# Kernel optimization log

Hardware: AMD Instinct MI355X
Metric: run time of the kernel (lower is better)

Reference implementation:

```python
import jax, jax.numpy as jnp
import numpy as np

N_LAYER, N_HEAD, N_EMBD, VOCAB, T_CTX, MAXT, B = 6, 8, 128, 18, 30, 2719, 64


def _ln(x, g, b, eps=1e-5):
    m = x.mean(-1, keepdims=True)
    v = ((x - m) ** 2).mean(-1, keepdims=True)
    return (x - m) * jax.lax.rsqrt(v + eps) * g + b


def setup_inputs() -> dict:
    key = jax.random.key(0)
    ks = iter(jax.random.split(key, 64))
    nrm = lambda shape: jax.random.normal(next(ks), shape, jnp.float32) * 0.02
    E, L4 = N_EMBD, 4 * N_EMBD
    inp = dict(
        states=jax.random.normal(next(ks), (B, T_CTX, 4, 84, 84), jnp.float32),
        actions=jax.random.randint(next(ks), (B, T_CTX, 1), 0, VOCAB),
        rtgs=jax.random.normal(next(ks), (B, T_CTX, 1), jnp.float32),
        timesteps=jax.random.randint(next(ks), (B, 1, 1), 0, MAXT),
        conv_w=nrm((E, 4, 84, 84)),
        class_tok=nrm((1, 1, E)),
        in_proj_w=nrm((3 * E, E)), in_proj_b=jnp.zeros(3 * E),
        out_w=nrm((E, E)), out_b=jnp.zeros(E),
        iln1_g=jnp.ones(E), iln1_b=jnp.zeros(E),
        iln2_g=jnp.ones(E), iln2_b=jnp.zeros(E),
        ffn_w1=nrm((E, E)), ffn_b1=jnp.zeros(E),
        ffn_w2=nrm((E, E)), ffn_b2=jnp.zeros(E),
        ret_w=nrm((E, 1)), ret_b=jnp.zeros(E),
        act_table=nrm((VOCAB, E)),
        pos_emb=nrm((1, 3 * T_CTX + 1, E)),
        global_pos_emb=nrm((1, MAXT + 1, E)),
        ln1_g=jnp.ones((N_LAYER, E)), ln1_b=jnp.zeros((N_LAYER, E)),
        Wq=nrm((N_LAYER, E, E)), bq=jnp.zeros((N_LAYER, E)),
        Wk=nrm((N_LAYER, E, E)), bk=jnp.zeros((N_LAYER, E)),
        Wv=nrm((N_LAYER, E, E)), bv=jnp.zeros((N_LAYER, E)),
        Wo=nrm((N_LAYER, E, E)), bo=jnp.zeros((N_LAYER, E)),
        ln2_g=jnp.ones((N_LAYER, E)), ln2_b=jnp.zeros((N_LAYER, E)),
        W1=nrm((N_LAYER, L4, E)), b1=jnp.zeros((N_LAYER, L4)),
        W2=nrm((N_LAYER, E, L4)), b2=jnp.zeros((N_LAYER, E)),
        lnf_g=jnp.ones(E), lnf_b=jnp.zeros(E),
        head_w=nrm((VOCAB, E)),
    )
    return inp


def _forward(states, actions, rtgs, timesteps, conv_w, class_tok, in_proj_w, in_proj_b,
             out_w, out_b, iln1_g, iln1_b, iln2_g, iln2_b, ffn_w1, ffn_b1, ffn_w2, ffn_b2,
             ret_w, ret_b, act_table, pos_emb, global_pos_emb,
             ln1_g, ln1_b, Wq, bq, Wk, bk, Wv, bv, Wo, bo, ln2_g, ln2_b,
             W1, b1, W2, b2, lnf_g, lnf_b, head_w):
    Bsz, T = states.shape[:2]
    E = conv_w.shape[0]
    H, hd = N_HEAD, E // N_HEAD
    # --- inner TIT: patch embed (kernel 84 = frame size -> single patch = one big dot) ---
    obs = states.reshape(Bsz * T, *states.shape[2:])                      # (BT,4,84,84)
    patch = jnp.einsum('bchw,echw->be', obs, conv_w)[:, None, :]          # (BT,1,E)
    x = jnp.concatenate([jnp.broadcast_to(class_tok, (Bsz * T, 1, E)), patch], axis=1)  # (BT,2,E)
    h = _ln(x, iln1_g, iln1_b)
    q, k, v = jnp.split(h @ in_proj_w.T + in_proj_b, 3, axis=-1)
    att = jax.nn.softmax(jnp.einsum('bqe,bke->bqk', q, k) / jnp.sqrt(jnp.float32(E)), axis=-1)
    x = x + jnp.einsum('bqk,bke->bqe', att, v) @ out_w.T + out_b
    h2 = _ln(x, iln2_g, iln2_b)
    x = x + jax.nn.relu(h2 @ ffn_w1.T + ffn_b1) @ ffn_w2.T + ffn_b2
    state_emb = x[:, 0, :].reshape(Bsz, T, E)                             # class token
    # --- token interleave (targets=None path -> length 3T-1, last T-1 actions) ---
    rtg_emb = jnp.tanh(rtgs @ ret_w.T + ret_b)                            # (B,T,E)
    act_emb = jnp.tanh(act_table[actions[..., 0]])                        # (B,T,E)
    Lt = 3 * T - 1
    tok = jnp.zeros((Bsz, Lt, E), states.dtype)
    tok = tok.at[:, 0::3].set(rtg_emb).at[:, 1::3].set(state_emb).at[:, 2::3].set(act_emb[:, 1:])
    pos = global_pos_emb[0][timesteps[:, 0, 0]][:, None, :] + pos_emb[:, :Lt, :]
    x = tok + pos
    # --- outer causal GPT blocks ---
    mask = jnp.tril(jnp.ones((Lt, Lt), bool))
    for i in range(N_LAYER):
        hh = _ln(x, ln1_g[i], ln1_b[i])
        proj = lambda w, b: (hh @ w.T + b).reshape(Bsz, Lt, H, hd).transpose(0, 2, 1, 3)
        q, k, v = proj(Wq[i], bq[i]), proj(Wk[i], bk[i]), proj(Wv[i], bv[i])
        att = jnp.einsum('bhqd,bhkd->bhqk', q, k) / jnp.sqrt(jnp.float32(hd))
        att = jax.nn.softmax(jnp.where(mask, att, -jnp.inf), axis=-1)
        y = jnp.einsum('bhqk,bhkd->bhqd', att, v).transpose(0, 2, 1, 3).reshape(Bsz, Lt, E)
        x = x + y @ Wo[i].T + bo[i]
        hh2 = _ln(x, ln2_g[i], ln2_b[i])
        x = x + jax.nn.gelu(hh2 @ W1[i].T + b1[i], approximate=False) @ W2[i].T + b2[i]
    logits = _ln(x, lnf_g, lnf_b) @ head_w.T
    return logits[:, 1::3, :]                                             # (B,T,vocab) state-position logits


def reference(states, actions, rtgs, timesteps, conv_w, class_tok, in_proj_w, in_proj_b,
              out_w, out_b, iln1_g, iln1_b, iln2_g, iln2_b, ffn_w1, ffn_b1, ffn_w2, ffn_b2,
              ret_w, ret_b, act_table, pos_emb, global_pos_emb,
              ln1_g, ln1_b, Wq, bq, Wk, bk, Wv, bv, Wo, bo, ln2_g, ln2_b,
              W1, b1, W2, b2, lnf_g, lnf_b, head_w):
    return _forward(states, actions, rtgs, timesteps, conv_w, class_tok, in_proj_w, in_proj_b,
                    out_w, out_b, iln1_g, iln1_b, iln2_g, iln2_b, ffn_w1, ffn_b1, ffn_w2, ffn_b2,
                    ret_w, ret_b, act_table, pos_emb, global_pos_emb,
                    ln1_g, ln1_b, Wq, bq, Wk, bk, Wv, bv, Wo, bo, ln2_g, ln2_b,
                    W1, b1, W2, b2, lnf_g, lnf_b, head_w)
```

## Files before the change

kernel.cpp:

```cpp
#include <hip/hip_runtime.h>

#define NB   64
#define NT   30
#define NBT  1920
#define EE   128
#define KP   28224
#define LTK  89
#define NS   5696
#define NLY  6
#define NV   18
#define NZ   21

typedef unsigned short ushort_t;
using bf16x8 = __attribute__((ext_vector_type(8))) short;
using us8    = __attribute__((ext_vector_type(8))) unsigned short;
using f32x4  = __attribute__((ext_vector_type(4))) float;
using f32x16 = __attribute__((ext_vector_type(16))) float;

__device__ inline ushort_t f2bf(float f){
  union { float f; unsigned u; } v; v.f = f;
  unsigned r = v.u + 0x7FFFu + ((v.u >> 16) & 1u);
  return (ushort_t)(r >> 16);
}

__global__ __launch_bounds__(256) void wcvt(
  const float* conv, const float* Wq, const float* Wk, const float* Wv,
  const float* Wo, const float* W1, const float* W2,
  const float* in_w, const float* out_w, const float* f1w, const float* f2w,
  const float* bq, const float* bk, const float* bv,
  ushort_t* dc, ushort_t* dqkv, ushort_t* dout, ushort_t* d1, ushort_t* d2,
  ushort_t* dinw, ushort_t* doutw, ushort_t* df1, ushort_t* df2, float* bqkv)
{
  if (blockIdx.x >= 4776){
    int idx = (blockIdx.x-4776)*256 + threadIdx.x;
    if (idx < NLY*128){ int l=idx>>7, j=idx&127;
      bqkv[l*384+j]=bq[idx]; bqkv[l*384+128+j]=bk[idx]; bqkv[l*384+256+j]=bv[idx]; }
    return;
  }
  long i = 4l*((long)blockIdx.x*256 + threadIdx.x);
  if (i >= 3612672l && i < 3907584l){
    long o = i - 3612672l;
    int  seg = (int)(o / 98304l);
    long off2 = o - (long)seg*98304l;
    long layer = off2 >> 14, rem = off2 & 16383l;
    const float* s = (seg==0) ? Wq : (seg==1) ? Wk : Wv;
    float4 f = *reinterpret_cast<const float4*>(s+off2);
    long dst = layer*49152l + (long)seg*16384l + rem;
    dqkv[dst]=f2bf(f.x); dqkv[dst+1]=f2bf(f.y); dqkv[dst+2]=f2bf(f.z); dqkv[dst+3]=f2bf(f.w);
    return;
  }
  const float* s; ushort_t* d; long off;
  if      (i < 3612672l){ s=conv;  d=dc;    off=i; }
  else if (i < 4005888l){ s=Wo;    d=dout;  off=i-3907584l; }
  else if (i < 4399104l){ s=W1;    d=d1;    off=i-4005888l; }
  else if (i < 4792320l){ s=W2;    d=d2;    off=i-4399104l; }
  else if (i < 4841472l){ s=in_w;  d=dinw;  off=i-4792320l; }
  else if (i < 4857856l){ s=out_w; d=doutw; off=i-4841472l; }
  else if (i < 4874240l){ s=f1w;   d=df1;   off=i-4857856l; }
  else                  { s=f2w;   d=df2;   off=i-4874240l; }
  float4 f = *reinterpret_cast<const float4*>(s+off);
  d[off]=f2bf(f.x); d[off+1]=f2bf(f.y); d[off+2]=f2bf(f.z); d[off+3]=f2bf(f.w);
}

__global__ __launch_bounds__(256) void patch_gemm(
  const float* __restrict__ A, const ushort_t* __restrict__ Wb, float* __restrict__ C)
{
  __shared__ __align__(16) ushort_t As[64*64];
  __shared__ __align__(16) ushort_t Ws[128*64];
  const int tid = threadIdx.x, lane = tid & 63, wid = tid >> 6;
  const int m0 = blockIdx.x * 64;
  const int kbase = blockIdx.z * 1344;
  float* Cz = C + (size_t)blockIdx.z * NBT * EE;
  const int ra = tid>>2, ca = (tid&3)*16, swa = (ra&7)<<3;
  const int rw = tid>>1, cw = (tid&1)*32, sww = (rw&7)<<3;
  const float*    Ab = A  + (size_t)(m0+ra)*KP + kbase + ca;
  const ushort_t* Wp = Wb + (size_t)rw*KP  + kbase + cw;
  f32x4 acc[8];
  #pragma unroll
  for (int j=0;j<8;j++) acc[j] = (f32x4){0.f,0.f,0.f,0.f};
  float4 fa[4]; us8 wr[4];
  #pragma unroll
  for (int q=0;q<4;q++) fa[q] = *reinterpret_cast<const float4*>(Ab + 4*q);
  #pragma unroll
  for (int q=0;q<4;q++) wr[q] = *reinterpret_cast<const us8*>(Wp + 8*q);

  for (int kt = 0; kt < 21; ++kt){
    { us8 o0, o1;
      o0[0]=f2bf(fa[0].x); o0[1]=f2bf(fa[0].y); o0[2]=f2bf(fa[0].z); o0[3]=f2bf(fa[0].w);
      o0[4]=f2bf(fa[1].x); o0[5]=f2bf(fa[1].y); o0[6]=f2bf(fa[1].z); o0[7]=f2bf(fa[1].w);
      o1[0]=f2bf(fa[2].x); o1[1]=f2bf(fa[2].y); o1[2]=f2bf(fa[2].z); o1[3]=f2bf(fa[2].w);
      o1[4]=f2bf(fa[3].x); o1[5]=f2bf(fa[3].y); o1[6]=f2bf(fa[3].z); o1[7]=f2bf(fa[3].w);
      *reinterpret_cast<us8*>(&As[ra*64 + ( ca    ^ swa)]) = o0;
      *reinterpret_cast<us8*>(&As[ra*64 + ((ca+8) ^ swa)]) = o1;
      #pragma unroll
      for (int q=0;q<4;q++)
        *reinterpret_cast<us8*>(&Ws[rw*64 + ((cw+8*q) ^ sww)]) = wr[q];
    }
    if (kt < 20){
      #pragma unroll
      for (int q=0;q<4;q++) fa[q] = *reinterpret_cast<const float4*>(Ab + (kt+1)*64 + 4*q);
      #pragma unroll
      for (int q=0;q<4;q++) wr[q] = *reinterpret_cast<const us8*>(Wp + (kt+1)*64 + 8*q);
    }
    __syncthreads();
    #pragma unroll
    for (int ks=0; ks<2; ++ks){
      int arow = wid*16 + (lane&15);
      int kb = ks*32 + (lane>>4)*8;
      bf16x8 a = *reinterpret_cast<const bf16x8*>(&As[arow*64 + (kb ^ ((arow&7)<<3))]);
      #pragma unroll
      for (int nt=0; nt<8; ++nt){
        int nn = nt*16 + (lane&15);
        bf16x8 b = *reinterpret_cast<const bf16x8*>(&Ws[nn*64 + (kb ^ ((nn&7)<<3))]);
        acc[nt] = __builtin_amdgcn_mfma_f32_16x16x32_bf16(a, b, acc[nt], 0,0,0);
      }
    }
    __syncthreads();
  }
  #pragma unroll
  for (int nt=0; nt<8; ++nt)
    #pragma unroll
    for (int rr=0;rr<4;rr++){
      int row = m0 + wid*16 + (lane>>4)*4 + rr;
      int col = nt*16 + (lane&15);
      Cz[row*EE + col] = acc[nt][rr];
    }
}

__global__ __launch_bounds__(256, 1) void inner_tit(
  const float* __restrict__ part, const float* __restrict__ ctok,
  const ushort_t* __restrict__ inw, const float* __restrict__ in_b,
  const ushort_t* __restrict__ outw, const float* __restrict__ out_b,
  const float* __restrict__ g1, const float* __restrict__ b1_,
  const float* __restrict__ g2, const float* __restrict__ b2_,
  const ushort_t* __restrict__ f1wb, const float* __restrict__ fb1,
  const ushort_t* __restrict__ f2wb, const float* __restrict__ fb2,
  const float* __restrict__ rtgs, const int* __restrict__ actions,
  const int* __restrict__ tsteps, const float* __restrict__ ret_w,
  const float* __restrict__ ret_b, const float* __restrict__ act_tab,
  const float* __restrict__ pos_emb, const float* __restrict__ gpos,
  const float* __restrict__ ln1g0, const float* __restrict__ ln1b0,
  float* __restrict__ x, ushort_t* __restrict__ xln)
{
  __shared__ __align__(16) ushort_t wbuf[384*128];
  __shared__ float xs[16*128];
  __shared__ __align__(16) ushort_t hb[16*128];
  __shared__ __align__(16) ushort_t hf[16*128];
  __shared__ float qkv[16*384];
  __shared__ float ssm[32];
  const int tid = threadIdx.x, lane = tid & 63, wid = tid >> 6;
  const int bt0 = blockIdx.x * 8;

  auto stageWB = [&](const ushort_t* src, int R, int rowoff){
    for (int c = tid; c < R*16; c += 256){
      int rr = c >> 4, cc = (c & 15) * 8;
      *reinterpret_cast<us8*>(&wbuf[(rowoff+rr)*128 + (cc ^ ((rr&7)<<3))]) =
        *reinterpret_cast<const us8*>(src + (size_t)rr*128 + cc);
    }
  };
  auto lnrow = [&](const float* gam, const float* bet, ushort_t* dst){
    int r = tid >> 4, e0 = (tid & 15) * 8;
    float v[8];
    #pragma unroll
    for (int j=0;j<8;j++) v[j] = xs[r*128 + e0 + j];
    float s = 0;
    #pragma unroll
    for (int j=0;j<8;j++) s += v[j];
    s += __shfl_xor(s,1); s += __shfl_xor(s,2); s += __shfl_xor(s,4); s += __shfl_xor(s,8);
    float mean = s * (1.0f/128.0f);
    float vs = 0;
    #pragma unroll
    for (int j=0;j<8;j++){ float d = v[j]-mean; vs += d*d; }
    vs += __shfl_xor(vs,1); vs += __shfl_xor(vs,2); vs += __shfl_xor(vs,4); vs += __shfl_xor(vs,8);
    float rstd = rsqrtf(vs*(1.0f/128.0f) + 1e-5f);
    us8 o;
    #pragma unroll
    for (int j=0;j<8;j++) o[j] = f2bf((v[j]-mean)*rstd*gam[e0+j] + bet[e0+j]);
    *reinterpret_cast<us8*>(&dst[r*128 + (e0 ^ ((r&7)<<3))]) = o;
  };

  { int r = tid >> 4, e0 = (tid & 15) * 8;
    float v[8];
    if ((r & 1) == 0){
      #pragma unroll
      for (int j=0;j<8;j++) v[j] = ctok[e0+j];
    } else {
      #pragma unroll
      for (int j=0;j<8;j++) v[j] = 0.f;
      int bt = bt0 + (r>>1);
      for (int z=0; z<NZ; ++z){
        const float* p = part + (size_t)z*NBT*EE + (size_t)bt*128 + e0;
        float4 f0 = *reinterpret_cast<const float4*>(p);
        float4 f1 = *reinterpret_cast<const float4*>(p+4);
        v[0]+=f0.x; v[1]+=f0.y; v[2]+=f0.z; v[3]+=f0.w;
        v[4]+=f1.x; v[5]+=f1.y; v[6]+=f1.z; v[7]+=f1.w;
      }
    }
    #pragma unroll
    for (int j=0;j<8;j++) xs[r*128 + e0 + j] = v[j];
  }
  stageWB(inw, 384, 0);
  __syncthreads();

  lnrow(g1, b1_, hb);
  __syncthreads();

  { int al = lane & 15, kq = (lane>>4)*8;
    #pragma unroll
    for (int j=0;j<6;++j){
      int nt = wid*6 + j;
      f32x4 acc = (f32x4){0.f,0.f,0.f,0.f};
      int nrow = nt*16 + al, nsw = (nrow&7)<<3;
      #pragma unroll
      for (int ks=0; ks<4; ++ks){
        int kb = ks*32 + kq;
        bf16x8 a = *reinterpret_cast<const bf16x8*>(&hb[al*128 + (kb ^ ((al&7)<<3))]);
        bf16x8 b = *reinterpret_cast<const bf16x8*>(&wbuf[nrow*128 + (kb ^ nsw)]);
        acc = __builtin_amdgcn_mfma_f32_16x16x32_bf16(a, b, acc, 0,0,0);
      }
      float bia = in_b[nt*16 + al];
      #pragma unroll
      for (int rr=0; rr<4; ++rr){
        int row = (lane>>4)*4 + rr;
        qkv[row*384 + nt*16 + al] = acc[rr] + bia;
      }
    }
  }
  __syncthreads();

  { int d = tid >> 3, j = tid & 7;
    int i = d >> 2, p = d & 3;
    const float* qp = &qkv[(2*i + (p>>1))*384 + j*16];
    const float* kp = &qkv[(2*i + (p&1))*384 + 128 + j*16];
    float s = 0;
    #pragma unroll
    for (int e=0;e<16;e++) s += qp[e]*kp[e];
    s += __shfl_xor(s,1); s += __shfl_xor(s,2); s += __shfl_xor(s,4);
    if (j == 0) ssm[d] = s;
  }
  stageWB(outw, 128, 0);
  stageWB(f1wb, 128, 128);
  stageWB(f2wb, 128, 256);
  __syncthreads();

  { int r = tid >> 4, e0 = (tid & 15)*8;
    int i = r >> 1, t = r & 1;
    const float sc = 0.08838834764831845f;
    float s0 = ssm[i*4 + t*2]*sc, s1 = ssm[i*4 + t*2 + 1]*sc;
    float m = fmaxf(s0,s1), p0 = __expf(s0-m), p1 = __expf(s1-m);
    float iv = 1.0f/(p0+p1); p0 *= iv; p1 *= iv;
    const float* v0 = &qkv[(2*i)*384 + 256 + e0];
    const float* v1 = &qkv[(2*i+1)*384 + 256 + e0];
    us8 o;
    #pragma unroll
    for (int j=0;j<8;j++) o[j] = f2bf(p0*v0[j] + p1*v1[j]);
    *reinterpret_cast<us8*>(&hb[r*128 + (e0 ^ ((r&7)<<3))]) = o;
  }
  __syncthreads();

  { int al = lane & 15, kq = (lane>>4)*8;
    #pragma unroll
    for (int j=0;j<2;++j){
      int nt = wid*2 + j;
      f32x4 acc = (f32x4){0.f,0.f,0.f,0.f};
      int nrow = nt*16 + al, nsw = (nrow&7)<<3;
      #pragma unroll
      for (int ks=0; ks<4; ++ks){
        int kb = ks*32 + kq;
        bf16x8 a = *reinterpret_cast<const bf16x8*>(&hb[al*128 + (kb ^ ((al&7)<<3))]);
        bf16x8 b = *reinterpret_cast<const bf16x8*>(&wbuf[nrow*128 + (kb ^ nsw)]);
        acc = __builtin_amdgcn_mfma_f32_16x16x32_bf16(a, b, acc, 0,0,0);
      }
      float bia = out_b[nt*16 + al];
      #pragma unroll
      for (int rr=0; rr<4; ++rr){
        int row = (lane>>4)*4 + rr;
        xs[row*128 + nt*16 + al] += acc[rr] + bia;
      }
    }
  }
  __syncthreads();

  lnrow(g2, b2_, hb);
  __syncthreads();

  { int al = lane & 15, kq = (lane>>4)*8;
    #pragma unroll
    for (int j=0;j<2;++j){
      int nt = wid*2 + j;
      f32x4 acc = (f32x4){0.f,0.f,0.f,0.f};
      int nrow = nt*16 + al, nsw = (nrow&7)<<3;
      #pragma unroll
      for (int ks=0; ks<4; ++ks){
        int kb = ks*32 + kq;
        bf16x8 a = *reinterpret_cast<const bf16x8*>(&hb[al*128 + (kb ^ ((al&7)<<3))]);
        bf16x8 b = *reinterpret_cast<const bf16x8*>(&wbuf[(128+nrow)*128 + (kb ^ nsw)]);
        acc = __builtin_amdgcn_mfma_f32_16x16x32_bf16(a, b, acc, 0,0,0);
      }
      float bia = fb1[nt*16 + al];
      #pragma unroll
      for (int rr=0; rr<4; ++rr){
        int row = (lane>>4)*4 + rr;
        hf[row*128 + ((nt*16+al) ^ ((row&7)<<3))] = f2bf(fmaxf(acc[rr] + bia, 0.f));
      }
    }
  }
  __syncthreads();

  { int al = lane & 15, kq = (lane>>4)*8;
    #pragma unroll
    for (int j=0;j<2;++j){
      int nt = wid*2 + j;
      f32x4 acc = (f32x4){0.f,0.f,0.f,0.f};
      int nrow = nt*16 + al, nsw = (nrow&7)<<3;
      #pragma unroll
      for (int ks=0; ks<4; ++ks){
        int kb = ks*32 + kq;
        bf16x8 a = *reinterpret_cast<const bf16x8*>(&hf[al*128 + (kb ^ ((al&7)<<3))]);
        bf16x8 b = *reinterpret_cast<const bf16x8*>(&wbuf[(256+nrow)*128 + (kb ^ nsw)]);
        acc = __builtin_amdgcn_mfma_f32_16x16x32_bf16(a, b, acc, 0,0,0);
      }
      float bia = fb2[nt*16 + al];
      #pragma unroll
      for (int rr=0; rr<4; ++rr){
        int row = (lane>>4)*4 + rr;
        xs[row*128 + nt*16 + al] += acc[rr] + bia;
      }
    }
  }
  __syncthreads();

  { int q = tid >> 3, j = tid & 7;
    if (q < 24){
      int i = q / 3, kind = q - 3*i;
      int btg = bt0 + i, b = btg / NT, t = btg - b*NT;
      bool valid = !(kind == 2 && t == 0);
      if (valid){
        int prow = (kind==0) ? 3*t : (kind==1) ? 3*t+1 : 3*t-1;
        size_t xrow = ((size_t)b*LTK + prow)*128;
        int ts = tsteps[b];
        int e0 = j*16;
        float v[16];
        if (kind == 1){
          #pragma unroll
          for (int e=0;e<16;e++) v[e] = xs[(2*i)*128 + e0 + e];
        } else if (kind == 0){
          float rv = rtgs[b*NT+t];
          #pragma unroll
          for (int e=0;e<16;e++) v[e] = tanhf(rv*ret_w[e0+e] + ret_b[e0+e]);
        } else {
          int a = actions[b*NT+t];
          #pragma unroll
          for (int e=0;e<16;e++) v[e] = tanhf(act_tab[a*128 + e0 + e]);
        }
        #pragma unroll
        for (int e=0;e<16;e++)
          v[e] += gpos[(size_t)ts*128 + e0 + e] + pos_emb[prow*128 + e0 + e];
        #pragma unroll
        for (int e=0;e<16;e++) x[xrow + e0 + e] = v[e];
        float s = 0;
        #pragma unroll
        for (int e=0;e<16;e++) s += v[e];
        s += __shfl_xor(s,1); s += __shfl_xor(s,2); s += __shfl_xor(s,4);
        float mean = s * (1.0f/128.0f);
        float vs = 0;
        #pragma unroll
        for (int e=0;e<16;e++){ float d = v[e]-mean; vs += d*d; }
        vs += __shfl_xor(vs,1); vs += __shfl_xor(vs,2); vs += __shfl_xor(vs,4);
        float rstd = rsqrtf(vs*(1.0f/128.0f) + 1e-5f);
        #pragma unroll
        for (int e=0;e<16;e++)
          xln[xrow + e0 + e] = f2bf((v[e]-mean)*rstd*ln1g0[e0+e] + ln1b0[e0+e]);
      }
    }
  }
}

__global__ __launch_bounds__(256, 2) void attn_fused(
  const ushort_t* __restrict__ xln, const ushort_t* __restrict__ Wqkv,
  const float* __restrict__ bqkv, ushort_t* __restrict__ y)
{
  __shared__ __align__(16) char sm[69504];
  ushort_t* ab  = (ushort_t*)sm;
  ushort_t* wb  = (ushort_t*)(sm + 24576);
  float*    S   = (float*)sm;
  ushort_t* qa  = (ushort_t*)(sm + 37248);
  ushort_t* ka  = (ushort_t*)(sm + 41472);
  ushort_t* vta = (ushort_t*)(sm + 45696);
  ushort_t* pb  = (ushort_t*)(sm + 49152);
  float*    inv = (float*)(sm + 69120);

  const int b = blockIdx.x >> 3, h = blockIdx.x & 7;
  const int tid = threadIdx.x, lane = tid & 63, wid = tid >> 6;

  for (int idx = tid; idx < 1536; idx += 256){
    int row = idx >> 4, c0 = (idx & 15) * 8;
    us8 v;
    if (row < LTK) v = *reinterpret_cast<const us8*>(xln + ((size_t)(b*LTK+row))*128 + c0);
    else           v = (us8){0,0,0,0,0,0,0,0};
    *reinterpret_cast<us8*>(&ab[row*128 + (c0 ^ ((row&7)<<3))]) = v;
  }
  for (int idx = tid; idx < 384; idx += 256){
    int rr = idx >> 3, c = (idx & 7) * 16;
    int seg = rr >> 4, n = rr & 15;
    const ushort_t* src = Wqkv + (size_t)(seg*128 + h*16 + n)*128 + c;
    int sw = (rr&7)<<3;
    *reinterpret_cast<us8*>(&wb[rr*128 + ( c    ^ sw)]) = *reinterpret_cast<const us8*>(src);
    *reinterpret_cast<us8*>(&wb[rr*128 + ((c+8) ^ sw)]) = *reinterpret_cast<const us8*>(src+8);
  }
  __syncthreads();

  for (int idx = wid; idx < 18; idx += 4){
    int rt = idx / 3, nt = idx - 3*(idx/3);
    f32x4 acc = (f32x4){0.f,0.f,0.f,0.f};
    int arow = rt*16 + (lane&15), asw = (arow&7)<<3;
    int nrow = nt*16 + (lane&15), nsw = (nrow&7)<<3;
    #pragma unroll
    for (int ks=0; ks<4; ++ks){
      int kb = ks*32 + (lane>>4)*8;
      bf16x8 a = *reinterpret_cast<const bf16x8*>(&ab[arow*128 + (kb ^ asw)]);
      bf16x8 bf = *reinterpret_cast<const bf16x8*>(&wb[nrow*128 + (kb ^ nsw)]);
      acc = __builtin_amdgcn_mfma_f32_16x16x32_bf16(a, bf, acc, 0,0,0);
    }
    int d = lane & 15;
    float bia = bqkv[nt*128 + h*16 + d];
    #pragma unroll
    for (int rr=0; rr<4; ++rr){
      int rg = rt*16 + (lane>>4)*4 + rr;
      ushort_t hv = f2bf(acc[rr] + bia);
      if      (nt == 0) qa[rg*22 + d] = hv;
      else if (nt == 1) ka[rg*22 + d] = hv;
      else              vta[d*108 + rg] = hv;
    }
  }
  __syncthreads();

  {
    static const int TR[6] = {0,1,1,2,2,2};
    static const int TC[6] = {0,0,1,0,1,2};
    for (int idx = wid; idx < 6; idx += 4){
      int R = TR[idx], C = TC[idx];
      int arow = R*32 + (lane&31), brow = C*32 + (lane&31);
      int ke = (lane>>5)*8;
      bf16x8 a  = *reinterpret_cast<const bf16x8*>(&qa[arow*22 + ke]);
      bf16x8 bf = *reinterpret_cast<const bf16x8*>(&ka[brow*22 + ke]);
      f32x16 sc = {};
      sc = __builtin_amdgcn_mfma_f32_32x32x16_bf16(a, bf, sc, 0,0,0);
      #pragma unroll
      for (int r=0; r<16; ++r){
        int rin = (r&3) + 8*(r>>2) + 4*(lane>>5);
        S[(R*32+rin)*97 + C*32 + (lane&31)] = sc[r]*0.25f;
      }
    }
  }
  __syncthreads();

  if (tid < 192){
    int t = tid >> 1, half = tid & 1;
    int u0 = half*48;
    float mx = -1e30f;
    if (t < LTK){
      for (int u=u0; u<u0+48; ++u) if (u<=t) mx = fmaxf(mx, S[t*97+u]);
    }
    mx = fmaxf(mx, __shfl_xor(mx,1));
    float smv = 0;
    if (t < LTK){
      for (int u=u0; u<u0+48; ++u){
        float p = 0;
        if (u<=t){ p = __expf(S[t*97+u]-mx); smv += p; }
        pb[t*104+u] = f2bf(p);
      }
    } else {
      for (int u=u0; u<u0+48; ++u) pb[t*104+u] = 0;
    }
    smv += __shfl_xor(smv,1);
    if (half==0) inv[t] = (t<LTK) ? 1.0f/smv : 0.0f;
  }
  __syncthreads();

  for (int rt = wid; rt < 6; rt += 4){
    int arow = rt*16 + (lane&15);
    f32x4 acc = (f32x4){0.f,0.f,0.f,0.f};
    #pragma unroll
    for (int ks=0; ks<3; ++ks){
      int kb = ks*32 + (lane>>4)*8;
      bf16x8 a  = *reinterpret_cast<const bf16x8*>(&pb[arow*104 + kb]);
      bf16x8 bf = *reinterpret_cast<const bf16x8*>(&vta[(lane&15)*108 + kb]);
      acc = __builtin_amdgcn_mfma_f32_16x16x32_bf16(a, bf, acc, 0,0,0);
    }
    #pragma unroll
    for (int rr=0; rr<4; ++rr){
      int rg = rt*16 + (lane>>4)*4 + rr;
      if (rg < LTK)
        y[(size_t)(b*LTK+rg)*128 + h*16 + (lane&15)] = f2bf(acc[rr]*inv[rg]);
    }
  }
}

template<bool HEAD>
__global__ __launch_bounds__(256, 2) void ffn_fused(
  const ushort_t* __restrict__ yg, const ushort_t* __restrict__ Wo,
  const float* __restrict__ bo, const float* __restrict__ g2,
  const float* __restrict__ b2g, const ushort_t* __restrict__ W1,
  const float* __restrict__ b1v, const ushort_t* __restrict__ W2,
  const float* __restrict__ b2v, float* __restrict__ x,
  const float* __restrict__ lnng, const float* __restrict__ lnnb,
  ushort_t* __restrict__ xlnout,
  const float* __restrict__ lnfg, const float* __restrict__ lnfb,
  const float* __restrict__ hw, float* __restrict__ out)
{
  __shared__ __align__(16) char sm[66304];
  ushort_t* wbs = (ushort_t*)sm;
  float*    xr  = (float*)(sm + 32768);
  ushort_t* h2  = (ushort_t*)(sm + 49664);
  ushort_t* f1  = (ushort_t*)(sm + 57856);
  const int tid = threadIdx.x, lane = tid & 63, wid = tid >> 6;
  const int m0 = blockIdx.x * 32;

  auto stageW = [&](const ushort_t* src_base, size_t stride, int buf){
    int rr = tid >> 2, q = tid & 3, sw = (rr&7)<<3;
    const ushort_t* s = src_base + (size_t)rr*stride + q*32;
    ushort_t* d = wbs + buf*8192 + rr*128;
    #pragma unroll
    for (int g=0; g<4; ++g)
      *reinterpret_cast<us8*>(&d[(q*32+g*8) ^ sw]) =
        *reinterpret_cast<const us8*>(s + g*8);
  };
  auto gemmT = [&](const ushort_t* abuf, int buf, f32x4* accp){
    int nrow = wid*16 + (lane&15), nsw = (nrow&7)<<3;
    const ushort_t* wbp = wbs + buf*8192;
    #pragma unroll
    for (int rt=0; rt<2; ++rt){
      int arow = rt*16 + (lane&15), asw = (arow&7)<<3;
      #pragma unroll
      for (int ks=0; ks<4; ++ks){
        int kb = ks*32 + (lane>>4)*8;
        bf16x8 a = *reinterpret_cast<const bf16x8*>(&abuf[arow*128 + (kb ^ asw)]);
        bf16x8 bb = *reinterpret_cast<const bf16x8*>(&wbp[nrow*128 + (kb ^ nsw)]);
        accp[rt] = __builtin_amdgcn_mfma_f32_16x16x32_bf16(a, bb, accp[rt], 0,0,0);
      }
    }
  };

  { int rr = tid>>3, q = tid&7, sw = (rr&7)<<3;
    const ushort_t* src = yg + (size_t)(m0+rr)*128 + q*16;
    *reinterpret_cast<us8*>(&f1[rr*128 + ((q*16)   ^ sw)]) = *reinterpret_cast<const us8*>(src);
    *reinterpret_cast<us8*>(&f1[rr*128 + ((q*16+8) ^ sw)]) = *reinterpret_cast<const us8*>(src+8);
  }
  stageW(Wo, 128, 0);
  __syncthreads();
  f32x4 accA[2][2];
  #pragma unroll
  for (int s_=0;s_<2;++s_){ accA[s_][0]=(f32x4){0,0,0,0}; accA[s_][1]=(f32x4){0,0,0,0}; }
  stageW(Wo + 64*128, 128, 1);
  gemmT(f1, 0, accA[0]);
  __syncthreads();
  gemmT(f1, 1, accA[1]);
  #pragma unroll
  for (int s_=0; s_<2; ++s_){
    int col = s_*64 + wid*16 + (lane&15);
    float bia = bo[col];
    #pragma unroll
    for (int rt=0; rt<2; ++rt)
      #pragma unroll
      for (int rr=0; rr<4; ++rr){
        int row = rt*16 + (lane>>4)*4 + rr;
        xr[row*132 + col] = accA[s_][rt][rr] + bia + x[(size_t)(m0+row)*128 + col];
      }
  }
  __syncthreads();

  { int r = tid>>3, q = tid&7;
    float xv[16];
    #pragma unroll
    for (int i=0;i<16;i++) xv[i] = xr[r*132 + q*16 + i];
    float s = 0;
    #pragma unroll
    for (int i=0;i<16;i++) s += xv[i];
    s += __shfl_xor(s,1); s += __shfl_xor(s,2); s += __shfl_xor(s,4);
    float mean = s * (1.0f/128.0f);
    float vs = 0;
    #pragma unroll
    for (int i=0;i<16;i++){ float d = xv[i]-mean; vs += d*d; }
    vs += __shfl_xor(vs,1); vs += __shfl_xor(vs,2); vs += __shfl_xor(vs,4);
    float rstd = rsqrtf(vs*(1.0f/128.0f) + 1e-5f);
    int sw = (r&7)<<3;
    #pragma unroll
    for (int g=0; g<2; ++g){
      us8 o;
      #pragma unroll
      for (int j=0;j<8;j++){
        int c = q*16 + g*8 + j;
        o[j] = f2bf((xv[g*8+j]-mean)*rstd*g2[c] + b2g[c]);
      }
      *reinterpret_cast<us8*>(&h2[r*128 + ((q*16+g*8) ^ sw)]) = o;
    }
  }
  stageW(W1, 128, 0);
  __syncthreads();

  f32x4 acc2[2][2];
  #pragma unroll
  for (int s_=0;s_<2;++s_){ acc2[s_][0]=(f32x4){0,0,0,0}; acc2[s_][1]=(f32x4){0,0,0,0}; }
  int buf = 0;
  for (int c=0; c<4; ++c){
    stageW(W1 + (size_t)(c*128+64)*128, 128, buf^1);
    { f32x4 ac[2] = {(f32x4){0,0,0,0},(f32x4){0,0,0,0}};
      gemmT(h2, buf, ac);
      int cl = wid*16 + (lane&15);
      float bia = b1v[c*128 + cl];
      #pragma unroll
      for (int rt=0; rt<2; ++rt)
        #pragma unroll
        for (int rr=0; rr<4; ++rr){
          int row = rt*16 + (lane>>4)*4 + rr;
          float v = ac[rt][rr] + bia;
          v = 0.5f*v*(1.0f + erff(v*0.70710678118654752f));
          f1[row*128 + (cl ^ ((row&7)<<3))] = f2bf(v);
        }
    }
    __syncthreads();
    stageW(W2 + (size_t)c*128, 512, buf);
    { f32x4 ac[2] = {(f32x4){0,0,0,0},(f32x4){0,0,0,0}};
      gemmT(h2, buf^1, ac);
      int cl = 64 + wid*16 + (lane&15);
      float bia = b1v[c*128 + cl];
      #pragma unroll
      for (int rt=0; rt<2; ++rt)
        #pragma unroll
        for (int rr=0; rr<4; ++rr){
          int row = rt*16 + (lane>>4)*4 + rr;
          float v = ac[rt][rr] + bia;
          v = 0.5f*v*(1.0f + erff(v*0.70710678118654752f));
          f1[row*128 + (cl ^ ((row&7)<<3))] = f2bf(v);
        }
    }
    __syncthreads();
    stageW(W2 + (size_t)64*512 + (size_t)c*128, 512, buf^1);
    gemmT(f1, buf, acc2[0]);
    __syncthreads();
    if (c < 3) stageW(W1 + (size_t)((c+1)*128)*128, 128, buf);
    gemmT(f1, buf^1, acc2[1]);
    __syncthreads();
  }

  #pragma unroll
  for (int s_=0; s_<2; ++s_){
    int col = s_*64 + wid*16 + (lane&15);
    float bia = b2v[col];
    #pragma unroll
    for (int rt=0; rt<2; ++rt)
      #pragma unroll
      for (int rr=0; rr<4; ++rr){
        int row = rt*16 + (lane>>4)*4 + rr;
        float v = acc2[s_][rt][rr] + bia + xr[row*132 + col];
        xr[row*132 + col] = v;
        if constexpr (!HEAD) x[(size_t)(m0+row)*128 + col] = v;
      }
  }
  __syncthreads();
  if constexpr (!HEAD){
    int r = tid>>3, q = tid&7;
    float xv[16];
    #pragma unroll
    for (int i=0;i<16;i++) xv[i] = xr[r*132 + q*16 + i];
    float s = 0;
    #pragma unroll
    for (int i=0;i<16;i++) s += xv[i];
    s += __shfl_xor(s,1); s += __shfl_xor(s,2); s += __shfl_xor(s,4);
    float mean = s * (1.0f/128.0f);
    float vs = 0;
    #pragma unroll
    for (int i=0;i<16;i++){ float d = xv[i]-mean; vs += d*d; }
    vs += __shfl_xor(vs,1); vs += __shfl_xor(vs,2); vs += __shfl_xor(vs,4);
    float rstd = rsqrtf(vs*(1.0f/128.0f) + 1e-5f);
    #pragma unroll
    for (int g=0; g<2; ++g){
      us8 o;
      #pragma unroll
      for (int j=0;j<8;j++){
        int c = q*16 + g*8 + j;
        o[j] = f2bf((xv[g*8+j]-mean)*rstd*lnng[c] + lnnb[c]);
      }
      *reinterpret_cast<us8*>(xlnout + (size_t)(m0+r)*128 + q*16 + g*8) = o;
    }
  } else {
    for (int r = wid; r < 32; r += 4){
      int s = m0 + r, b = s / LTK, p = s - b*LTK;
      if (p % 3 != 1) continue;
      int t = p / 3;
      float v1 = xr[r*132 + lane];
      float v2 = xr[r*132 + 64 + lane];
      float sum = v1 + v2;
      sum += __shfl_xor(sum,1); sum += __shfl_xor(sum,2); sum += __shfl_xor(sum,4);
      sum += __shfl_xor(sum,8); sum += __shfl_xor(sum,16); sum += __shfl_xor(sum,32);
      float mean = sum*(1.0f/128.0f);
      float d1 = v1-mean, d2 = v2-mean;
      float var = d1*d1 + d2*d2;
      var += __shfl_xor(var,1); var += __shfl_xor(var,2); var += __shfl_xor(var,4);
      var += __shfl_xor(var,8); var += __shfl_xor(var,16); var += __shfl_xor(var,32);
      float rstd = rsqrtf(var*(1.0f/128.0f) + 1e-5f);
      float h1 = d1*rstd*lnfg[lane]    + lnfb[lane];
      float h2v= d2*rstd*lnfg[lane+64] + lnfb[lane+64];
      #pragma unroll
      for (int o=0; o<NV; ++o){
        float sdot = h1*hw[o*128+lane] + h2v*hw[o*128+lane+64];
        sdot += __shfl_xor(sdot,1); sdot += __shfl_xor(sdot,2); sdot += __shfl_xor(sdot,4);
        sdot += __shfl_xor(sdot,8); sdot += __shfl_xor(sdot,16); sdot += __shfl_xor(sdot,32);
        if (lane == 0) out[(size_t)(b*NT+t)*NV + o] = sdot;
      }
    }
  }
}

extern "C" void kernel_launch(void* const* d_in, const int* in_sizes, int n_in,
                              void* d_out, int out_size, void* d_ws, size_t ws_size,
                              hipStream_t stream)
{
  const float* states  = (const float*)d_in[0];
  const int*   actions = (const int*)  d_in[1];
  const float* rtgs    = (const float*)d_in[2];
  const int*   tsteps  = (const int*)  d_in[3];
  const float* conv_w  = (const float*)d_in[4];
  const float* ctok    = (const float*)d_in[5];
  const float* in_w    = (const float*)d_in[6];
  const float* in_b    = (const float*)d_in[7];
  const float* out_w   = (const float*)d_in[8];
  const float* out_b   = (const float*)d_in[9];
  const float* i1g     = (const float*)d_in[10];
  const float* i1b     = (const float*)d_in[11];
  const float* i2g     = (const float*)d_in[12];
  const float* i2b     = (const float*)d_in[13];
  const float* fw1     = (const float*)d_in[14];
  const float* fb1     = (const float*)d_in[15];
  const float* fw2     = (const float*)d_in[16];
  const float* fb2     = (const float*)d_in[17];
  const float* ret_w   = (const float*)d_in[18];
  const float* ret_b   = (const float*)d_in[19];
  const float* act_tab = (const float*)d_in[20];
  const float* pos_emb = (const float*)d_in[21];
  const float* gpos    = (const float*)d_in[22];
  const float* ln1g    = (const float*)d_in[23];
  const float* ln1b    = (const float*)d_in[24];
  const float* Wq      = (const float*)d_in[25];
  const float* bq      = (const float*)d_in[26];
  const float* Wk      = (const float*)d_in[27];
  const float* bk      = (const float*)d_in[28];
  const float* Wv      = (const float*)d_in[29];
  const float* bv      = (const float*)d_in[30];
  const float* Wo      = (const float*)d_in[31];
  const float* bo      = (const float*)d_in[32];
  const float* ln2g    = (const float*)d_in[33];
  const float* ln2b    = (const float*)d_in[34];
  const float* W1      = (const float*)d_in[35];
  const float* b1      = (const float*)d_in[36];
  const float* W2      = (const float*)d_in[37];
  const float* b2      = (const float*)d_in[38];
  const float* lnfg    = (const float*)d_in[39];
  const float* lnfb    = (const float*)d_in[40];
  const float* head_w  = (const float*)d_in[41];

  char* w = (char*)d_ws;
  size_t off = 0;
  auto alloc = [&](size_t bytes)->char* {
    char* p = w + off; off += (bytes + 255) & ~(size_t)255; return p;
  };
  float*    part  = (float*)   alloc((size_t)NZ*NBT*EE*4);
  float*    x     = (float*)   alloc((size_t)NS*EE*4);
  ushort_t* xln   = (ushort_t*)alloc((size_t)NS*EE*2);
  ushort_t* yb    = (ushort_t*)alloc((size_t)NS*EE*2);
  ushort_t* cwb   = (ushort_t*)alloc((size_t)EE*KP*2);
  ushort_t* Wqkvb = (ushort_t*)alloc((size_t)NLY*384*128*2);
  ushort_t* Wob   = (ushort_t*)alloc((size_t)NLY*128*128*2);
  ushort_t* W1b   = (ushort_t*)alloc((size_t)NLY*512*128*2);
  ushort_t* W2b   = (ushort_t*)alloc((size_t)NLY*128*512*2);
  ushort_t* inwb  = (ushort_t*)alloc((size_t)384*128*2);
  ushort_t* outwb = (ushort_t*)alloc((size_t)128*128*2);
  ushort_t* f1wb  = (ushort_t*)alloc((size_t)128*128*2);
  ushort_t* f2wb  = (ushort_t*)alloc((size_t)128*128*2);
  float*    bqkv  = (float*)   alloc(NLY*384*4);
  (void)in_sizes; (void)n_in; (void)out_size; (void)ws_size;

  wcvt<<<4779,256,0,stream>>>(conv_w,Wq,Wk,Wv,Wo,W1,W2,
                              in_w,out_w,fw1,fw2, bq,bk,bv,
                              cwb,Wqkvb,Wob,W1b,W2b,
                              inwb,outwb,f1wb,f2wb, bqkv);
  patch_gemm<<<dim3(30,1,NZ),256,0,stream>>>(states, cwb, part);
  inner_tit<<<240,256,0,stream>>>(part, ctok, inwb, in_b, outwb, out_b,
                                  i1g,i1b,i2g,i2b, f1wb,fb1, f2wb,fb2,
                                  rtgs, actions, tsteps, ret_w, ret_b, act_tab,
                                  pos_emb, gpos, ln1g, ln1b, x, xln);
  for (int i=0;i<NLY;i++){
    attn_fused<<<512,256,0,stream>>>(
      xln, Wqkvb+(size_t)i*49152, bqkv+(size_t)i*384, yb);
    if (i < NLY-1)
      ffn_fused<false><<<178,256,0,stream>>>(
        yb, Wob+(size_t)i*16384, bo+i*128, ln2g+i*128, ln2b+i*128,
        W1b+(size_t)i*65536, b1+i*512, W2b+(size_t)i*65536, b2+i*128, x,
        ln1g+(i+1)*128, ln1b+(i+1)*128, xln,
        nullptr, nullptr, nullptr, nullptr);
    else
      ffn_fused<true><<<178,256,0,stream>>>(
        yb, Wob+(size_t)i*16384, bo+i*128, ln2g+i*128, ln2b+i*128,
        W1b+(size_t)i*65536, b1+i*512, W2b+(size_t)i*65536, b2+i*128, x,
        nullptr, nullptr, nullptr,
        lnfg, lnfb, head_w, (float*)d_out);
  }
}
```

Measured before the change: 341.8 us.

## Fuse attention and FFN into one per-layer kernel with ping-pong LN buffers

```diff
diff --git a/kernel.cpp b/kernel.cpp
--- a/kernel.cpp
+++ b/kernel.cpp
@@ -376,151 +376,151 @@
   }
 }
 
-__global__ __launch_bounds__(256, 2) void attn_fused(
-  const ushort_t* __restrict__ xln, const ushort_t* __restrict__ Wqkv,
-  const float* __restrict__ bqkv, ushort_t* __restrict__ y)
-{
-  __shared__ __align__(16) char sm[69504];
-  ushort_t* ab  = (ushort_t*)sm;
-  ushort_t* wb  = (ushort_t*)(sm + 24576);
-  float*    S   = (float*)sm;
-  ushort_t* qa  = (ushort_t*)(sm + 37248);
-  ushort_t* ka  = (ushort_t*)(sm + 41472);
-  ushort_t* vta = (ushort_t*)(sm + 45696);
-  ushort_t* pb  = (ushort_t*)(sm + 49152);
-  float*    inv = (float*)(sm + 69120);
-
-  const int b = blockIdx.x >> 3, h = blockIdx.x & 7;
-  const int tid = threadIdx.x, lane = tid & 63, wid = tid >> 6;
-
-  for (int idx = tid; idx < 1536; idx += 256){
-    int row = idx >> 4, c0 = (idx & 15) * 8;
-    us8 v;
-    if (row < LTK) v = *reinterpret_cast<const us8*>(xln + ((size_t)(b*LTK+row))*128 + c0);
-    else           v = (us8){0,0,0,0,0,0,0,0};
-    *reinterpret_cast<us8*>(&ab[row*128 + (c0 ^ ((row&7)<<3))]) = v;
-  }
-  for (int idx = tid; idx < 384; idx += 256){
-    int rr = idx >> 3, c = (idx & 7) * 16;
-    int seg = rr >> 4, n = rr & 15;
-    const ushort_t* src = Wqkv + (size_t)(seg*128 + h*16 + n)*128 + c;
-    int sw = (rr&7)<<3;
-    *reinterpret_cast<us8*>(&wb[rr*128 + ( c    ^ sw)]) = *reinterpret_cast<const us8*>(src);
-    *reinterpret_cast<us8*>(&wb[rr*128 + ((c+8) ^ sw)]) = *reinterpret_cast<const us8*>(src+8);
-  }
-  __syncthreads();
-
-  for (int idx = wid; idx < 18; idx += 4){
-    int rt = idx / 3, nt = idx - 3*(idx/3);
-    f32x4 acc = (f32x4){0.f,0.f,0.f,0.f};
-    int arow = rt*16 + (lane&15), asw = (arow&7)<<3;
-    int nrow = nt*16 + (lane&15), nsw = (nrow&7)<<3;
-    #pragma unroll
-    for (int ks=0; ks<4; ++ks){
-      int kb = ks*32 + (lane>>4)*8;
-      bf16x8 a = *reinterpret_cast<const bf16x8*>(&ab[arow*128 + (kb ^ asw)]);
-      bf16x8 bf = *reinterpret_cast<const bf16x8*>(&wb[nrow*128 + (kb ^ nsw)]);
-      acc = __builtin_amdgcn_mfma_f32_16x16x32_bf16(a, bf, acc, 0,0,0);
-    }
-    int d = lane & 15;
-    float bia = bqkv[nt*128 + h*16 + d];
-    #pragma unroll
-    for (int rr=0; rr<4; ++rr){
-      int rg = rt*16 + (lane>>4)*4 + rr;
-      ushort_t hv = f2bf(acc[rr] + bia);
-      if      (nt == 0) qa[rg*22 + d] = hv;
-      else if (nt == 1) ka[rg*22 + d] = hv;
-      else              vta[d*108 + rg] = hv;
-    }
-  }
-  __syncthreads();
-
-  {
-    static const int TR[6] = {0,1,1,2,2,2};
-    static const int TC[6] = {0,0,1,0,1,2};
-    for (int idx = wid; idx < 6; idx += 4){
-      int R = TR[idx], C = TC[idx];
-      int arow = R*32 + (lane&31), brow = C*32 + (lane&31);
-      int ke = (lane>>5)*8;
-      bf16x8 a  = *reinterpret_cast<const bf16x8*>(&qa[arow*22 + ke]);
-      bf16x8 bf = *reinterpret_cast<const bf16x8*>(&ka[brow*22 + ke]);
-      f32x16 sc = {};
-      sc = __builtin_amdgcn_mfma_f32_32x32x16_bf16(a, bf, sc, 0,0,0);
-      #pragma unroll
-      for (int r=0; r<16; ++r){
-        int rin = (r&3) + 8*(r>>2) + 4*(lane>>5);
-        S[(R*32+rin)*97 + C*32 + (lane&31)] = sc[r]*0.25f;
-      }
-    }
-  }
-  __syncthreads();
-
-  if (tid < 192){
-    int t = tid >> 1, half = tid & 1;
-    int u0 = half*48;
-    float mx = -1e30f;
-    if (t < LTK){
-      for (int u=u0; u<u0+48; ++u) if (u<=t) mx = fmaxf(mx, S[t*97+u]);
-    }
-    mx = fmaxf(mx, __shfl_xor(mx,1));
-    float smv = 0;
-    if (t < LTK){
-      for (int u=u0; u<u0+48; ++u){
-        float p = 0;
-        if (u<=t){ p = __expf(S[t*97+u]-mx); smv += p; }
-        pb[t*104+u] = f2bf(p);
-      }
-    } else {
-      for (int u=u0; u<u0+48; ++u) pb[t*104+u] = 0;
-    }
-    smv += __shfl_xor(smv,1);
-    if (half==0) inv[t] = (t<LTK) ? 1.0f/smv : 0.0f;
-  }
-  __syncthreads();
-
-  for (int rt = wid; rt < 6; rt += 4){
-    int arow = rt*16 + (lane&15);
-    f32x4 acc = (f32x4){0.f,0.f,0.f,0.f};
-    #pragma unroll
-    for (int ks=0; ks<3; ++ks){
-      int kb = ks*32 + (lane>>4)*8;
-      bf16x8 a  = *reinterpret_cast<const bf16x8*>(&pb[arow*104 + kb]);
-      bf16x8 bf = *reinterpret_cast<const bf16x8*>(&vta[(lane&15)*108 + kb]);
-      acc = __builtin_amdgcn_mfma_f32_16x16x32_bf16(a, bf, acc, 0,0,0);
-    }
-    #pragma unroll
-    for (int rr=0; rr<4; ++rr){
-      int rg = rt*16 + (lane>>4)*4 + rr;
-      if (rg < LTK)
-        y[(size_t)(b*LTK+rg)*128 + h*16 + (lane&15)] = f2bf(acc[rr]*inv[rg]);
-    }
-  }
-}
-
 template<bool HEAD>
-__global__ __launch_bounds__(256, 2) void ffn_fused(
-  const ushort_t* __restrict__ yg, const ushort_t* __restrict__ Wo,
-  const float* __restrict__ bo, const float* __restrict__ g2,
-  const float* __restrict__ b2g, const ushort_t* __restrict__ W1,
-  const float* __restrict__ b1v, const ushort_t* __restrict__ W2,
-  const float* __restrict__ b2v, float* __restrict__ x,
+__global__ __launch_bounds__(256, 2) void layer_fused(
+  const ushort_t* __restrict__ xln, float* __restrict__ x,
+  const ushort_t* __restrict__ Wqkv, const float* __restrict__ bqkv,
+  const ushort_t* __restrict__ Wo, const float* __restrict__ bo,
+  const float* __restrict__ g2, const float* __restrict__ b2g,
+  const ushort_t* __restrict__ W1, const float* __restrict__ b1v,
+  const ushort_t* __restrict__ W2, const float* __restrict__ b2v,
   const float* __restrict__ lnng, const float* __restrict__ lnnb,
   ushort_t* __restrict__ xlnout,
   const float* __restrict__ lnfg, const float* __restrict__ lnfb,
   const float* __restrict__ hw, float* __restrict__ out)
 {
-  __shared__ __align__(16) char sm[66304];
-  ushort_t* wbs = (ushort_t*)sm;
+  __shared__ __align__(16) char sm[73088];
+  ushort_t* kln = (ushort_t*)sm;
+  ushort_t* wb  = (ushort_t*)(sm + 24576);
+  ushort_t* qa  = (ushort_t*)(sm + 36864);
+  ushort_t* ka  = (ushort_t*)(sm + 38272);
+  ushort_t* vta = (ushort_t*)(sm + 42496);
+  float*    S   = (float*)(sm + 45824);
+  ushort_t* pb  = (ushort_t*)(sm + 58112);
+  float*    inv = (float*)(sm + 64768);
+  ushort_t* yb  = (ushort_t*)(sm + 64896);
+  ushort_t* wdb = (ushort_t*)sm;
   float*    xr  = (float*)(sm + 32768);
   ushort_t* h2  = (ushort_t*)(sm + 49664);
-  ushort_t* f1  = (ushort_t*)(sm + 57856);
+  ushort_t* f1  = (ushort_t*)(sm + 64896);
+
   const int tid = threadIdx.x, lane = tid & 63, wid = tid >> 6;
-  const int m0 = blockIdx.x * 32;
+  const int b = blockIdx.x / 3, j = blockIdx.x % 3;
+  const int R0 = j*32;
+  const int P  = (j==2) ? LTK : R0 + 32;
+  const int SR = R0 + 32;
+  const int PT16 = (P+15)>>4, PT32 = (P+31)>>5;
+  const int VR = (j==2) ? (LTK-64) : 32;
+  const int m0g = b*LTK + R0;
+
+  for (int idx = tid; idx < SR*16; idx += 256){
+    int row = idx >> 4, c0 = (idx & 15)*8;
+    us8 v;
+    if (row < LTK) v = *reinterpret_cast<const us8*>(xln + ((size_t)(b*LTK+row))*128 + c0);
+    else           v = (us8){0,0,0,0,0,0,0,0};
+    *reinterpret_cast<us8*>(&kln[row*128 + (c0 ^ ((row&7)<<3))]) = v;
+  }
+  __syncthreads();
+
+  for (int h = 0; h < 8; ++h){
+    for (int idx = tid; idx < 384; idx += 256){
+      int rr = idx >> 3, c = (idx & 7)*16;
+      int seg = rr >> 4, n = rr & 15;
+      const ushort_t* src = Wqkv + (size_t)(seg*128 + h*16 + n)*128 + c;
+      int sw = (rr&7)<<3;
+      *reinterpret_cast<us8*>(&wb[rr*128 + ( c    ^ sw)]) = *reinterpret_cast<const us8*>(src);
+      *reinterpret_cast<us8*>(&wb[rr*128 + ((c+8) ^ sw)]) = *reinterpret_cast<const us8*>(src+8);
+    }
+    __syncthreads();
+    { int NU = 2 + 2*PT16;
+      for (int u = wid; u < NU; u += 4){
+        int typ, rt;
+        if (u < 2)            { typ = 0; rt = u; }
+        else if (u < 2+PT16)  { typ = 1; rt = u-2; }
+        else                  { typ = 2; rt = u-2-PT16; }
+        int al = lane & 15;
+        int arow = ((typ==0)? R0 : 0) + rt*16 + al;
+        int asw = (arow&7)<<3;
+        int nrow = typ*16 + al, nsw = (nrow&7)<<3;
+        f32x4 acc = (f32x4){0.f,0.f,0.f,0.f};
+        #pragma unroll
+        for (int ks=0; ks<4; ++ks){
+          int kb = ks*32 + (lane>>4)*8;
+          bf16x8 a  = *reinterpret_cast<const bf16x8*>(&kln[arow*128 + (kb ^ asw)]);
+          bf16x8 bf = *reinterpret_cast<const bf16x8*>(&wb[nrow*128 + (kb ^ nsw)]);
+          acc = __builtin_amdgcn_mfma_f32_16x16x32_bf16(a, bf, acc, 0,0,0);
+        }
+        float bia = bqkv[typ*128 + h*16 + al];
+        #pragma unroll
+        for (int rr=0; rr<4; ++rr){
+          int rg = rt*16 + (lane>>4)*4 + rr;
+          ushort_t hv = f2bf(acc[rr] + bia);
+          if      (typ == 0) qa[rg*22 + al] = hv;
+          else if (typ == 1) ka[rg*22 + al] = hv;
+          else               vta[al*104 + rg] = hv;
+        }
+      }
+    }
+    __syncthreads();
+    for (int ct = wid; ct < PT32; ct += 4){
+      int ke = (lane>>5)*8;
+      bf16x8 a  = *reinterpret_cast<const bf16x8*>(&qa[(lane&31)*22 + ke]);
+      bf16x8 bf = *reinterpret_cast<const bf16x8*>(&ka[(ct*32+(lane&31))*22 + ke]);
+      f32x16 sc = {};
+      sc = __builtin_amdgcn_mfma_f32_32x32x16_bf16(a, bf, sc, 0,0,0);
+      #pragma unroll
+      for (int r=0; r<16; ++r){
+        int rin = (r&3) + 8*(r>>2) + 4*(lane>>5);
+        S[rin*96 + ct*32 + (lane&31)] = sc[r]*0.25f;
+      }
+    }
+    __syncthreads();
+    { int r = tid >> 3, q8 = tid & 7;
+      int tg = R0 + r, u0 = q8*12, lim = PT32*32;
+      float sv[12];
+      float mx = -1e30f;
+      #pragma unroll
+      for (int k=0;k<12;k++){
+        int u = u0+k;
+        float s = (u < lim && u <= tg) ? S[r*96+u] : -1e30f;
+        sv[k] = s; mx = fmaxf(mx, s);
+      }
+      mx = fmaxf(mx, __shfl_xor(mx,1));
+      mx = fmaxf(mx, __shfl_xor(mx,2));
+      mx = fmaxf(mx, __shfl_xor(mx,4));
+      float sum = 0;
+      #pragma unroll
+      for (int k=0;k<12;k++){
+        float p = (sv[k] > -1e29f) ? __expf(sv[k]-mx) : 0.f;
+        sum += p;
+        pb[r*104 + u0 + k] = f2bf(p);
+      }
+      sum += __shfl_xor(sum,1); sum += __shfl_xor(sum,2); sum += __shfl_xor(sum,4);
+      if (q8 == 0) inv[r] = 1.0f/sum;
+    }
+    __syncthreads();
+    for (int rt = wid; rt < 2; rt += 4){
+      int arow = rt*16 + (lane&15);
+      f32x4 acc = (f32x4){0.f,0.f,0.f,0.f};
+      for (int ks=0; ks<PT32; ++ks){
+        int kb = ks*32 + (lane>>4)*8;
+        bf16x8 a  = *reinterpret_cast<const bf16x8*>(&pb[arow*104 + kb]);
+        bf16x8 bf = *reinterpret_cast<const bf16x8*>(&vta[(lane&15)*104 + kb]);
+        acc = __builtin_amdgcn_mfma_f32_16x16x32_bf16(a, bf, acc, 0,0,0);
+      }
+      #pragma unroll
+      for (int rr=0; rr<4; ++rr){
+        int row = rt*16 + (lane>>4)*4 + rr;
+        yb[row*128 + ((h*16+(lane&15)) ^ ((row&7)<<3))] = f2bf(acc[rr]*inv[row]);
+      }
+    }
+    __syncthreads();
+  }
 
   auto stageW = [&](const ushort_t* src_base, size_t stride, int buf){
     int rr = tid >> 2, q = tid & 3, sw = (rr&7)<<3;
     const ushort_t* s = src_base + (size_t)rr*stride + q*32;
-    ushort_t* d = wbs + buf*8192 + rr*128;
+    ushort_t* d = wdb + buf*8192 + rr*128;
     #pragma unroll
     for (int g=0; g<4; ++g)
       *reinterpret_cast<us8*>(&d[(q*32+g*8) ^ sw]) =
@@ -528,34 +528,29 @@
   };
   auto gemmT = [&](const ushort_t* abuf, int buf, f32x4* accp){
     int nrow = wid*16 + (lane&15), nsw = (nrow&7)<<3;
-    const ushort_t* wbp = wbs + buf*8192;
+    const ushort_t* wbp = wdb + buf*8192;
     #pragma unroll
     for (int rt=0; rt<2; ++rt){
       int arow = rt*16 + (lane&15), asw = (arow&7)<<3;
       #pragma unroll
       for (int ks=0; ks<4; ++ks){
         int kb = ks*32 + (lane>>4)*8;
-        bf16x8 a = *reinterpret_cast<const bf16x8*>(&abuf[arow*128 + (kb ^ asw)]);
+        bf16x8 a  = *reinterpret_cast<const bf16x8*>(&abuf[arow*128 + (kb ^ asw)]);
         bf16x8 bb = *reinterpret_cast<const bf16x8*>(&wbp[nrow*128 + (kb ^ nsw)]);
         accp[rt] = __builtin_amdgcn_mfma_f32_16x16x32_bf16(a, bb, accp[rt], 0,0,0);
       }
     }
   };
 
-  { int rr = tid>>3, q = tid&7, sw = (rr&7)<<3;
-    const ushort_t* src = yg + (size_t)(m0+rr)*128 + q*16;
-    *reinterpret_cast<us8*>(&f1[rr*128 + ((q*16)   ^ sw)]) = *reinterpret_cast<const us8*>(src);
-    *reinterpret_cast<us8*>(&f1[rr*128 + ((q*16+8) ^ sw)]) = *reinterpret_cast<const us8*>(src+8);
-  }
   stageW(Wo, 128, 0);
   __syncthreads();
   f32x4 accA[2][2];
   #pragma unroll
   for (int s_=0;s_<2;++s_){ accA[s_][0]=(f32x4){0,0,0,0}; accA[s_][1]=(f32x4){0,0,0,0}; }
   stageW(Wo + 64*128, 128, 1);
-  gemmT(f1, 0, accA[0]);
-  __syncthreads();
-  gemmT(f1, 1, accA[1]);
+  gemmT(yb, 0, accA[0]);
+  __syncthreads();
+  gemmT(yb, 1, accA[1]);
   #pragma unroll
   for (int s_=0; s_<2; ++s_){
     int col = s_*64 + wid*16 + (lane&15);
@@ -565,7 +560,8 @@
       #pragma unroll
       for (int rr=0; rr<4; ++rr){
         int row = rt*16 + (lane>>4)*4 + rr;
-        xr[row*132 + col] = accA[s_][rt][rr] + bia + x[(size_t)(m0+row)*128 + col];
+        float xv_in = (row < VR) ? x[(size_t)(m0g+row)*128 + col] : 0.f;
+        xr[row*132 + col] = accA[s_][rt][rr] + bia + xv_in;
       }
   }
   __syncthreads();
@@ -589,9 +585,9 @@
     for (int g=0; g<2; ++g){
       us8 o;
       #pragma unroll
-      for (int j=0;j<8;j++){
-        int c = q*16 + g*8 + j;
-        o[j] = f2bf((xv[g*8+j]-mean)*rstd*g2[c] + b2g[c]);
+      for (int jj=0;jj<8;jj++){
+        int c = q*16 + g*8 + jj;
+        o[jj] = f2bf((xv[g*8+jj]-mean)*rstd*g2[c] + b2g[c]);
       }
       *reinterpret_cast<us8*>(&h2[r*128 + ((q*16+g*8) ^ sw)]) = o;
     }
@@ -655,38 +651,42 @@
         int row = rt*16 + (lane>>4)*4 + rr;
         float v = acc2[s_][rt][rr] + bia + xr[row*132 + col];
         xr[row*132 + col] = v;
-        if constexpr (!HEAD) x[(size_t)(m0+row)*128 + col] = v;
+        if constexpr (!HEAD){
+          if (row < VR) x[(size_t)(m0g+row)*128 + col] = v;
+        }
       }
   }
   __syncthreads();
   if constexpr (!HEAD){
     int r = tid>>3, q = tid&7;
-    float xv[16];
-    #pragma unroll
-    for (int i=0;i<16;i++) xv[i] = xr[r*132 + q*16 + i];
-    float s = 0;
-    #pragma unroll
-    for (int i=0;i<16;i++) s += xv[i];
-    s += __shfl_xor(s,1); s += __shfl_xor(s,2); s += __shfl_xor(s,4);
-    float mean = s * (1.0f/128.0f);
-    float vs = 0;
-    #pragma unroll
-    for (int i=0;i<16;i++){ float d = xv[i]-mean; vs += d*d; }
-    vs += __shfl_xor(vs,1); vs += __shfl_xor(vs,2); vs += __shfl_xor(vs,4);
-    float rstd = rsqrtf(vs*(1.0f/128.0f) + 1e-5f);
-    #pragma unroll
-    for (int g=0; g<2; ++g){
-      us8 o;
-      #pragma unroll
-      for (int j=0;j<8;j++){
-        int c = q*16 + g*8 + j;
-        o[j] = f2bf((xv[g*8+j]-mean)*rstd*lnng[c] + lnnb[c]);
-      }
-      *reinterpret_cast<us8*>(xlnout + (size_t)(m0+r)*128 + q*16 + g*8) = o;
+    if (r < VR){
+      float xv[16];
+      #pragma unroll
+      for (int i=0;i<16;i++) xv[i] = xr[r*132 + q*16 + i];
+      float s = 0;
+      #pragma unroll
+      for (int i=0;i<16;i++) s += xv[i];
+      s += __shfl_xor(s,1); s += __shfl_xor(s,2); s += __shfl_xor(s,4);
+      float mean = s * (1.0f/128.0f);
+      float vs = 0;
+      #pragma unroll
+      for (int i=0;i<16;i++){ float d = xv[i]-mean; vs += d*d; }
+      vs += __shfl_xor(vs,1); vs += __shfl_xor(vs,2); vs += __shfl_xor(vs,4);
+      float rstd = rsqrtf(vs*(1.0f/128.0f) + 1e-5f);
+      #pragma unroll
+      for (int g=0; g<2; ++g){
+        us8 o;
+        #pragma unroll
+        for (int jj=0;jj<8;jj++){
+          int c = q*16 + g*8 + jj;
+          o[jj] = f2bf((xv[g*8+jj]-mean)*rstd*lnng[c] + lnnb[c]);
+        }
+        *reinterpret_cast<us8*>(xlnout + (size_t)(m0g+r)*128 + q*16 + g*8) = o;
+      }
     }
   } else {
-    for (int r = wid; r < 32; r += 4){
-      int s = m0 + r, b = s / LTK, p = s - b*LTK;
+    for (int r = wid; r < VR; r += 4){
+      int s = m0g + r, bb2 = s / LTK, p = s - bb2*LTK;
       if (p % 3 != 1) continue;
       int t = p / 3;
       float v1 = xr[r*132 + lane];
@@ -707,7 +707,7 @@
         float sdot = h1*hw[o*128+lane] + h2v*hw[o*128+lane+64];
         sdot += __shfl_xor(sdot,1); sdot += __shfl_xor(sdot,2); sdot += __shfl_xor(sdot,4);
         sdot += __shfl_xor(sdot,8); sdot += __shfl_xor(sdot,16); sdot += __shfl_xor(sdot,32);
-        if (lane == 0) out[(size_t)(b*NT+t)*NV + o] = sdot;
+        if (lane == 0) out[(size_t)(bb2*NT+t)*NV + o] = sdot;
       }
     }
   }
@@ -767,8 +767,8 @@
   };
   float*    part  = (float*)   alloc((size_t)NZ*NBT*EE*4);
   float*    x     = (float*)   alloc((size_t)NS*EE*4);
-  ushort_t* xln   = (ushort_t*)alloc((size_t)NS*EE*2);
-  ushort_t* yb    = (ushort_t*)alloc((size_t)NS*EE*2);
+  ushort_t* xlnA  = (ushort_t*)alloc((size_t)NS*EE*2);
+  ushort_t* xlnB  = (ushort_t*)alloc((size_t)NS*EE*2);
   ushort_t* cwb   = (ushort_t*)alloc((size_t)EE*KP*2);
   ushort_t* Wqkvb = (ushort_t*)alloc((size_t)NLY*384*128*2);
   ushort_t* Wob   = (ushort_t*)alloc((size_t)NLY*128*128*2);
@@ -789,20 +789,22 @@
   inner_tit<<<240,256,0,stream>>>(part, ctok, inwb, in_b, outwb, out_b,
                                   i1g,i1b,i2g,i2b, f1wb,fb1, f2wb,fb2,
                                   rtgs, actions, tsteps, ret_w, ret_b, act_tab,
-                                  pos_emb, gpos, ln1g, ln1b, x, xln);
+                                  pos_emb, gpos, ln1g, ln1b, x, xlnA);
   for (int i=0;i<NLY;i++){
-    attn_fused<<<512,256,0,stream>>>(
-      xln, Wqkvb+(size_t)i*49152, bqkv+(size_t)i*384, yb);
+    ushort_t* xin  = (i & 1) ? xlnB : xlnA;
+    ushort_t* xout = (i & 1) ? xlnA : xlnB;
     if (i < NLY-1)
-      ffn_fused<false><<<178,256,0,stream>>>(
-        yb, Wob+(size_t)i*16384, bo+i*128, ln2g+i*128, ln2b+i*128,
-        W1b+(size_t)i*65536, b1+i*512, W2b+(size_t)i*65536, b2+i*128, x,
-        ln1g+(i+1)*128, ln1b+(i+1)*128, xln,
+      layer_fused<false><<<192,256,0,stream>>>(
+        xin, x, Wqkvb+(size_t)i*49152, bqkv+(size_t)i*384,
+        Wob+(size_t)i*16384, bo+i*128, ln2g+i*128, ln2b+i*128,
+        W1b+(size_t)i*65536, b1+i*512, W2b+(size_t)i*65536, b2+i*128,
+        ln1g+(i+1)*128, ln1b+(i+1)*128, xout,
         nullptr, nullptr, nullptr, nullptr);
     else
-      ffn_fused<true><<<178,256,0,stream>>>(
-        yb, Wob+(size_t)i*16384, bo+i*128, ln2g+i*128, ln2b+i*128,
-        W1b+(size_t)i*65536, b1+i*512, W2b+(size_t)i*65536, b2+i*128, x,
+      layer_fused<true><<<192,256,0,stream>>>(
+        xin, x, Wqkvb+(size_t)i*49152, bqkv+(size_t)i*384,
+        Wob+(size_t)i*16384, bo+i*128, ln2g+i*128, ln2b+i*128,
+        W1b+(size_t)i*65536, b1+i*512, W2b+(size_t)i*65536, b2+i*128,
         nullptr, nullptr, nullptr,
         lnfg, lnfb, head_w, (float*)d_out);
   }
```

Measured after the change: 393.0 us. +15.0%, slower.
